# Optimization experiments

Hardware: AMD Instinct MI355X
Metric: run time of the kernel (lower is better)

The kernel has to match this reference:

```python
import jax, jax.numpy as jnp
import numpy as np

N, E, IN_DIM, HID, HEADS, OUT_DIM = 50000, 800000, 256, 32, 8, 64
NEG_SLOPE = 0.2  # PyG GATConv default


def segment_softmax(logits, seg, num_segments):
    # logits: [E, H], seg: [E] destination node ids. Self-loops guarantee no empty segment.
    m = jnp.full((num_segments, logits.shape[1]), -jnp.inf, logits.dtype).at[seg].max(logits)
    e = jnp.exp(logits - m[seg])
    s = jnp.zeros((num_segments, logits.shape[1]), logits.dtype).at[seg].add(e)
    return e / s[seg]


def gat_conv(x, src, dst, W, a_src, a_dst, b, heads, out_ch, concat):
    n = x.shape[0]
    h = (x @ W).reshape(n, heads, out_ch)                      # [N,H,C]
    alpha_src = jnp.einsum('nhc,hc->nh', h, a_src)             # [N,H]
    alpha_dst = jnp.einsum('nhc,hc->nh', h, a_dst)             # [N,H]
    logits = jax.nn.leaky_relu(alpha_src[src] + alpha_dst[dst], NEG_SLOPE)  # [E,H]
    alpha = segment_softmax(logits, dst, n)                    # [E,H]
    msg = alpha[:, :, None] * h[src]                           # [E,H,C]
    out = jnp.zeros((n, heads, out_ch), x.dtype).at[dst].add(msg)
    out = out.reshape(n, heads * out_ch) if concat else out.mean(axis=1)
    return out + b


def setup_inputs() -> dict:
    key = jax.random.key(0)
    ks = jax.random.split(key, 10)
    x = jax.random.normal(ks[0], (N, IN_DIM), dtype=jnp.float32)
    edge_index = jax.random.randint(ks[1], (2, E), 0, N, dtype=jnp.int64)
    s1 = 1.0 / np.sqrt(IN_DIM)
    s2 = 1.0 / np.sqrt(HID * HEADS)
    return {
        'x': x,
        'edge_index': edge_index,
        'W1': jax.random.normal(ks[2], (IN_DIM, HEADS * HID), dtype=jnp.float32) * s1,
        'a_src1': jax.random.normal(ks[3], (HEADS, HID), dtype=jnp.float32) * s1,
        'a_dst1': jax.random.normal(ks[4], (HEADS, HID), dtype=jnp.float32) * s1,
        'b1': jnp.zeros((HEADS * HID,), dtype=jnp.float32),
        'W2': jax.random.normal(ks[5], (HEADS * HID, OUT_DIM), dtype=jnp.float32) * s2,
        'a_src2': jax.random.normal(ks[6], (1, OUT_DIM), dtype=jnp.float32) * s2,
        'a_dst2': jax.random.normal(ks[7], (1, OUT_DIM), dtype=jnp.float32) * s2,
        'b2': jnp.zeros((OUT_DIM,), dtype=jnp.float32),
    }


def reference(x, edge_index, W1, a_src1, a_dst1, b1, W2, a_src2, a_dst2, b2):
    # add self-loops (PyG GATConv default add_self_loops=True)
    loops = jnp.arange(N, dtype=edge_index.dtype)
    src = jnp.concatenate([edge_index[0], loops])
    dst = jnp.concatenate([edge_index[1], loops])
    h = gat_conv(x, src, dst, W1, a_src1, a_dst1, b1, HEADS, HID, True)
    h = jax.nn.elu(h)  # dropout identity in eval mode
    out = gat_conv(h, src, dst, W2, a_src2, a_dst2, b2, 1, OUT_DIM, False)
    return out
```

## Files before the change

kernel.cpp:

```cpp
#include <hip/hip_runtime.h>
#include <hip/hip_bf16.h>

static constexpr int HEADS = 8;
static constexpr int D1 = 256;
static constexpr int ODIM = 64;
static constexpr float NEG = 0.2f;

typedef __attribute__((ext_vector_type(8))) short bf16x8;
typedef __attribute__((ext_vector_type(8))) unsigned short u16x8;
typedef __attribute__((ext_vector_type(4))) float f32x4;

__device__ __forceinline__ float lrelu(float x) { return fmaxf(x, NEG * x); }
__device__ __forceinline__ float elu1(float x) { return x > 0.f ? x : expm1f(x); }

__device__ __forceinline__ unsigned short f2bf(float f) {
  unsigned u = __float_as_uint(f);
  unsigned r = (u + 0x7fffu + ((u >> 16) & 1u)) >> 16;
  return (unsigned short)r;
}
__device__ __forceinline__ float bf2f(unsigned short h) {
  return __uint_as_float((unsigned)h << 16);
}

__device__ __forceinline__ void gload_lds16(const void* g, void* l) {
  __builtin_amdgcn_global_load_lds(
      (const __attribute__((address_space(1))) void*)g,
      (__attribute__((address_space(3))) void*)l, 16, 0, 0);
}

__global__ void k_hist_prep(const int* __restrict__ dst, int E, int TE,
                            int* __restrict__ deg, int* __restrict__ erank,
                            const float* __restrict__ W1, const float* __restrict__ W2,
                            unsigned short* __restrict__ BT1, unsigned short* __restrict__ B2T,
                            int HB) {
  int b = blockIdx.x;
  if (b < HB) {
    int i = b * 256 + threadIdx.x;
    if (i < TE) {
      int d = (i < E) ? dst[i] : (i - E);
      erank[i] = atomicAdd(&deg[d], 1);
    }
  } else {
    int t = (b - HB) * 256 + threadIdx.x;
    if (t < 65536) {
      int k = t >> 8, nn = t & 255;
      BT1[nn * 256 + k] = f2bf(W1[t]);
    } else if (t < 65536 + 16384) {
      int t2 = t - 65536;
      int k = t2 >> 6, nn = t2 & 63;
      B2T[nn * 256 + k] = f2bf(W2[t2]);
    }
  }
}

__global__ void k_scan_lb(const int* __restrict__ deg, int n, int TE,
                          int* __restrict__ offs,
                          int* __restrict__ tstate, int* __restrict__ ticket) {
  __shared__ int sm[256];
  __shared__ int sh[2];
  if (threadIdx.x == 0) sh[0] = atomicAdd(ticket, 1);
  __syncthreads();
  const int tile = sh[0];
  int i = tile * 256 + threadIdx.x;
  int v = (i < n) ? deg[i] : 0;
  sm[threadIdx.x] = v;
  __syncthreads();
  for (int off = 1; off < 256; off <<= 1) {
    int t = (threadIdx.x >= off) ? sm[threadIdx.x - off] : 0;
    __syncthreads();
    sm[threadIdx.x] += t;
    __syncthreads();
  }
  const int total = sm[255];
  if (threadIdx.x == 0) {
    if (tile == 0) {
      __hip_atomic_store(&tstate[0], (2 << 24) | total, __ATOMIC_RELEASE,
                         __HIP_MEMORY_SCOPE_AGENT);
      sh[1] = 0;
    } else {
      __hip_atomic_store(&tstate[tile], (1 << 24) | total, __ATOMIC_RELEASE,
                         __HIP_MEMORY_SCOPE_AGENT);
    }
  }
  __syncthreads();
  if (tile != 0) {
    if (threadIdx.x < 64) {
      const int lane = threadIdx.x;
      int running = 0;
      int wstart = tile - 1;
      for (;;) {
        int idx = wstart - lane;
        int st = (idx >= 0)
                     ? __hip_atomic_load(&tstate[idx], __ATOMIC_ACQUIRE,
                                         __HIP_MEMORY_SCOPE_AGENT)
                     : (2 << 24);
        if (__ballot(st == 0)) continue;
        unsigned long long pref = __ballot((st >> 24) == 2);
        int contrib;
        if (pref) {
          int flane = (int)__ffsll(pref) - 1;
          contrib = (lane <= flane) ? (st & 0xFFFFFF) : 0;
        } else {
          contrib = st & 0xFFFFFF;
        }
#pragma unroll
        for (int off2 = 1; off2 < 64; off2 <<= 1) contrib += __shfl_xor(contrib, off2);
        running += contrib;
        if (pref) break;
        wstart -= 64;
      }
      if (lane == 0) {
        sh[1] = running;
        __hip_atomic_store(&tstate[tile], (2 << 24) | (running + total),
                           __ATOMIC_RELEASE, __HIP_MEMORY_SCOPE_AGENT);
      }
    }
    __syncthreads();
  }
  const int base = sh[1];
  if (i < n) offs[i] = base + sm[threadIdx.x] - v;
  if (i == 0) offs[n] = TE;
}

__global__ __launch_bounds__(512) void k_gemm1s(
    const float* __restrict__ X,
    const unsigned short* __restrict__ BT,
    const float* __restrict__ a_src, const float* __restrict__ a_dst,
    unsigned short* __restrict__ h1b,
    float* __restrict__ asrc, float* __restrict__ adst,
    int M, int Mblk,
    const int* __restrict__ src, const int* __restrict__ dst, int E, int TE,
    const int* __restrict__ offs, const int* __restrict__ erank,
    int* __restrict__ csr_src) {
  __shared__ __align__(128) char As[16384];
  __shared__ __align__(128) char Bs[32768];
  if (blockIdx.x >= Mblk) {
    int i = (blockIdx.x - Mblk) * 512 + threadIdx.x;
    if (i < TE) {
      int s, d;
      if (i < E) { s = src[i]; d = dst[i]; } else { s = i - E; d = i - E; }
      csr_src[offs[d] + erank[i]] = s;
    }
    return;
  }
  const int tid = threadIdx.x;
  const int lane = tid & 63;
  const int wid = tid >> 6;
  const int bm = blockIdx.x * 128;
  const int wm = wid >> 2, wn = wid & 3;
  f32x4 acc[4][4] = {};
  float4 xv[2][2];
  auto loadX = [&](int kb) {
#pragma unroll
    for (int q = 0; q < 2; ++q) {
      int c = q * 512 + tid;
      int r = c >> 3, kc = c & 7;
      int gr = bm + r;
      xv[q][0] = make_float4(0.f, 0.f, 0.f, 0.f);
      xv[q][1] = xv[q][0];
      if (gr < M) {
        xv[q][0] = *(const float4*)&X[(size_t)gr * 256 + kb + kc * 8];
        xv[q][1] = *(const float4*)&X[(size_t)gr * 256 + kb + kc * 8 + 4];
      }
    }
  };
  loadX(0);
  for (int kb = 0; kb < 256; kb += 64) {
#pragma unroll
    for (int q = 0; q < 2; ++q) {
      int c = q * 512 + tid;
      int r = c >> 3, kc = c & 7;
      float vv[8] = {xv[q][0].x, xv[q][0].y, xv[q][0].z, xv[q][0].w,
                     xv[q][1].x, xv[q][1].y, xv[q][1].z, xv[q][1].w};
      u16x8 hv;
#pragma unroll
      for (int j = 0; j < 8; ++j) hv[j] = f2bf(vv[j]);
      *(u16x8*)(As + r * 128 + ((kc * 16) ^ ((r & 7) << 4))) = hv;
    }
#pragma unroll
    for (int q = 0; q < 4; ++q) {
      int c = q * 512 + tid;
      int col = c >> 3;
      int b = ((c & 7) * 16) ^ ((col & 7) << 4);
      gload_lds16(BT + (size_t)col * 256 + kb + (b >> 1),
                  Bs + (size_t)(q * 512 + (tid & ~63)) * 16);
    }
    __syncthreads();
    if (kb + 64 < 256) loadX(kb + 64);
#pragma unroll
    for (int ks = 0; ks < 2; ++ks) {
      bf16x8 af[4], bfr[4];
      int bb = ks * 64 + (lane >> 4) * 16;
#pragma unroll
      for (int mi = 0; mi < 4; ++mi) {
        int row = wm * 64 + mi * 16 + (lane & 15);
        af[mi] = *(const bf16x8*)(As + row * 128 + (bb ^ ((row & 7) << 4)));
      }
#pragma unroll
      for (int ni = 0; ni < 4; ++ni) {
        int col = wn * 64 + ni * 16 + (lane & 15);
        bfr[ni] = *(const bf16x8*)(Bs + col * 128 + (bb ^ ((col & 7) << 4)));
      }
#pragma unroll
      for (int mi = 0; mi < 4; ++mi)
#pragma unroll
        for (int ni = 0; ni < 4; ++ni)
          acc[mi][ni] = __builtin_amdgcn_mfma_f32_16x16x32_bf16(af[mi], bfr[ni],
                                                                acc[mi][ni], 0, 0, 0);
    }
    __syncthreads();
  }
  const int h0 = 2 * wn, h1h = 2 * wn + 1;
  const int cl = lane & 15;
  const float as0 = a_src[h0 * 32 + cl],      ad0 = a_dst[h0 * 32 + cl];
  const float as1 = a_src[h0 * 32 + 16 + cl], ad1 = a_dst[h0 * 32 + 16 + cl];
  const float as2 = a_src[h1h * 32 + cl],      ad2 = a_dst[h1h * 32 + cl];
  const float as3 = a_src[h1h * 32 + 16 + cl], ad3 = a_dst[h1h * 32 + 16 + cl];
#pragma unroll
  for (int mi = 0; mi < 4; ++mi) {
    int gr0 = bm + wm * 64 + mi * 16 + (lane >> 4) * 4;
#pragma unroll
    for (int j = 0; j < 4; ++j) {
      int gr = gr0 + j;
#pragma unroll
      for (int ni = 0; ni < 4; ++ni) {
        int gc = wn * 64 + ni * 16 + cl;
        if (gr < M) h1b[(size_t)gr * 256 + gc] = f2bf(acc[mi][ni][j]);
      }
      float ps0 = acc[mi][0][j] * as0 + acc[mi][1][j] * as1;
      float pd0 = acc[mi][0][j] * ad0 + acc[mi][1][j] * ad1;
      float ps1 = acc[mi][2][j] * as2 + acc[mi][3][j] * as3;
      float pd1 = acc[mi][2][j] * ad2 + acc[mi][3][j] * ad3;
#pragma unroll
      for (int off = 1; off < 16; off <<= 1) {
        ps0 += __shfl_xor(ps0, off);
        pd0 += __shfl_xor(pd0, off);
        ps1 += __shfl_xor(ps1, off);
        pd1 += __shfl_xor(pd1, off);
      }
      if (cl == 0 && gr < M) {
        asrc[gr * 8 + h0] = ps0;
        adst[gr * 8 + h0] = pd0;
        asrc[gr * 8 + h1h] = ps1;
        adst[gr * 8 + h1h] = pd1;
      }
    }
  }
}

__global__ __launch_bounds__(512) void k_gemm2(
    const unsigned short* __restrict__ A,
    const unsigned short* __restrict__ B2T,
    const float* __restrict__ a_src, const float* __restrict__ a_dst,
    unsigned short* __restrict__ C,
    float* __restrict__ asrc, float* __restrict__ adst,
    int M) {
  __shared__ __align__(128) char As[16384];
  __shared__ __align__(128) char Bs[8192];
  __shared__ float red[2][128][2];
  const int tid = threadIdx.x;
  const int lane = tid & 63;
  const int wid = tid >> 6;
  const int bm = blockIdx.x * 128;
  const int wm = wid >> 1, wn = wid & 1;
  f32x4 acc[2][2] = {};
  for (int kb = 0; kb < 256; kb += 64) {
#pragma unroll
    for (int q = 0; q < 2; ++q) {
      int c = q * 512 + tid;
      int r = c >> 3;
      int b = ((c & 7) * 16) ^ ((r & 7) << 4);
      gload_lds16(A + (size_t)(bm + r) * 256 + kb + (b >> 1),
                  As + (size_t)(q * 512 + (tid & ~63)) * 16);
    }
    {
      int c = tid;
      int col = c >> 3;
      int b = ((c & 7) * 16) ^ ((col & 7) << 4);
      gload_lds16(B2T + (size_t)col * 256 + kb + (b >> 1),
                  Bs + (size_t)(tid & ~63) * 16);
    }
    __syncthreads();
#pragma unroll
    for (int ks = 0; ks < 2; ++ks) {
      bf16x8 af[2], bfr[2];
      int bb = ks * 64 + (lane >> 4) * 16;
#pragma unroll
      for (int mi = 0; mi < 2; ++mi) {
        int row = wm * 32 + mi * 16 + (lane & 15);
        af[mi] = *(const bf16x8*)(As + row * 128 + (bb ^ ((row & 7) << 4)));
      }
#pragma unroll
      for (int ni = 0; ni < 2; ++ni) {
        int col = wn * 32 + ni * 16 + (lane & 15);
        bfr[ni] = *(const bf16x8*)(Bs + col * 128 + (bb ^ ((col & 7) << 4)));
      }
#pragma unroll
      for (int mi = 0; mi < 2; ++mi)
#pragma unroll
        for (int ni = 0; ni < 2; ++ni)
          acc[mi][ni] = __builtin_amdgcn_mfma_f32_16x16x32_bf16(af[mi], bfr[ni],
                                                                acc[mi][ni], 0, 0, 0);
    }
    __syncthreads();
  }
  const int cl = lane & 15;
  const float a_s0 = a_src[wn * 32 + cl],      a_d0 = a_dst[wn * 32 + cl];
  const float a_s1 = a_src[wn * 32 + 16 + cl], a_d1 = a_dst[wn * 32 + 16 + cl];
#pragma unroll
  for (int mi = 0; mi < 2; ++mi) {
    int rl0 = wm * 32 + mi * 16 + (lane >> 4) * 4;
#pragma unroll
    for (int j = 0; j < 4; ++j) {
      int rl = rl0 + j;
      int gr = bm + rl;
#pragma unroll
      for (int ni = 0; ni < 2; ++ni) {
        int gc = wn * 32 + ni * 16 + cl;
        if (gr < M) C[(size_t)gr * 64 + gc] = f2bf(acc[mi][ni][j]);
      }
      float ps = acc[mi][0][j] * a_s0 + acc[mi][1][j] * a_s1;
      float pd = acc[mi][0][j] * a_d0 + acc[mi][1][j] * a_d1;
#pragma unroll
      for (int off = 1; off < 16; off <<= 1) {
        ps += __shfl_xor(ps, off);
        pd += __shfl_xor(pd, off);
      }
      if (cl == 0) {
        red[wn][rl][0] = ps;
        red[wn][rl][1] = pd;
      }
    }
  }
  __syncthreads();
  if (tid < 128) {
    int gr = bm + tid;
    if (gr < M) {
      asrc[gr] = red[0][tid][0] + red[1][tid][0];
      adst[gr] = red[0][tid][1] + red[1][tid][1];
    }
  }
}

__global__ void k_agg1(const int* __restrict__ offs, const int* __restrict__ csr_src,
                       const unsigned short* __restrict__ h1b, const float* __restrict__ asrc,
                       const float* __restrict__ adst, const float* __restrict__ b1,
                       int n, unsigned short* __restrict__ helu) {
  int wave = (blockIdx.x * blockDim.x + threadIdx.x) >> 6;
  int lane = threadIdx.x & 63;
  if (wave >= n) return;
  int wv = __builtin_amdgcn_readfirstlane(wave);
  const int es = lane >> 5;
  const int cg = lane & 31;
  const int hh = cg >> 2;
  float ad = adst[wv * 8 + hh];
  int b = offs[wv], e2 = offs[wv + 1];
  float ssum = 0.f;
  float acc[8] = {};
  int i = b;
  for (; i + 7 < e2; i += 8) {
    int s[4];
#pragma unroll
    for (int u = 0; u < 4; ++u) s[u] = csr_src[i + 2 * u + es];
    u16x8 r[4];
    float as_[4];
#pragma unroll
    for (int u = 0; u < 4; ++u) {
      r[u] = *(const u16x8*)&h1b[(size_t)s[u] * D1 + cg * 8];
      as_[u] = asrc[s[u] * 8 + hh];
    }
#pragma unroll
    for (int u = 0; u < 4; ++u) {
      float w = __expf(lrelu(as_[u] + ad));
      ssum += w;
#pragma unroll
      for (int j = 0; j < 8; ++j) acc[j] += w * bf2f(r[u][j]);
    }
  }
  for (; i < e2; i += 2) {
    int idx = i + es;
    bool act = idx < e2;
    int s = csr_src[act ? idx : e2 - 1];
    u16x8 r = *(const u16x8*)&h1b[(size_t)s * D1 + cg * 8];
    float w = act ? __expf(lrelu(asrc[s * 8 + hh] + ad)) : 0.f;
    ssum += w;
#pragma unroll
    for (int j = 0; j < 8; ++j) acc[j] += w * bf2f(r[j]);
  }
  ssum += __shfl_xor(ssum, 32);
#pragma unroll
  for (int j = 0; j < 8; ++j) acc[j] += __shfl_xor(acc[j], 32);
  if (lane < 32) {
    float rr = 1.f / ssum;
    float4 bb0 = *(const float4*)&b1[cg * 8];
    float4 bb1 = *(const float4*)&b1[cg * 8 + 4];
    float bbv[8] = {bb0.x, bb0.y, bb0.z, bb0.w, bb1.x, bb1.y, bb1.z, bb1.w};
    u16x8 o;
#pragma unroll
    for (int j = 0; j < 8; ++j) o[j] = f2bf(elu1(acc[j] * rr + bbv[j]));
    *(u16x8*)&helu[(size_t)wave * D1 + cg * 8] = o;
  }
}

__global__ void k_agg2(const int* __restrict__ offs, const int* __restrict__ csr_src,
                       const unsigned short* __restrict__ h2b, const float* __restrict__ asrc,
                       const float* __restrict__ adst, const float* __restrict__ b2,
                       int n, float* __restrict__ out) {
  int wave = (blockIdx.x * blockDim.x + threadIdx.x) >> 6;
  int lane = threadIdx.x & 63;
  if (wave >= n) return;
  int wv = __builtin_amdgcn_readfirstlane(wave);
  float ad = adst[wv];
  int b = offs[wv], e2 = offs[wv + 1];
  const int es = lane >> 3;
  const int cg = lane & 7;
  float ssum = 0.f;
  float acc[8] = {};
  int i = b;
  for (; i + 15 < e2; i += 16) {
    int s0 = csr_src[i + es], s1 = csr_src[i + 8 + es];
    u16x8 r0 = *(const u16x8*)&h2b[(size_t)s0 * ODIM + cg * 8];
    u16x8 r1 = *(const u16x8*)&h2b[(size_t)s1 * ODIM + cg * 8];
    float a0 = asrc[s0], a1 = asrc[s1];
    float w0 = __expf(lrelu(a0 + ad));
    float w1 = __expf(lrelu(a1 + ad));
    ssum += w0 + w1;
#pragma unroll
    for (int j = 0; j < 8; ++j) acc[j] += w0 * bf2f(r0[j]) + w1 * bf2f(r1[j]);
  }
  for (; i < e2; i += 8) {
    int idx = i + es;
    bool act = idx < e2;
    int s = csr_src[act ? idx : e2 - 1];
    u16x8 r = *(const u16x8*)&h2b[(size_t)s * ODIM + cg * 8];
    float w = act ? __expf(lrelu(asrc[s] + ad)) : 0.f;
    ssum += w;
#pragma unroll
    for (int j = 0; j < 8; ++j) acc[j] += w * bf2f(r[j]);
  }
#pragma unroll
  for (int off = 8; off < 64; off <<= 1) {
    ssum += __shfl_xor(ssum, off);
#pragma unroll
    for (int j = 0; j < 8; ++j) acc[j] += __shfl_xor(acc[j], off);
  }
  if (lane < 8) {
    float r = 1.f / ssum;
    float4 bb0 = *(const float4*)&b2[cg * 8];
    float4 bb1 = *(const float4*)&b2[cg * 8 + 4];
    float4 o0, o1;
    o0.x = acc[0] * r + bb0.x; o0.y = acc[1] * r + bb0.y;
    o0.z = acc[2] * r + bb0.z; o0.w = acc[3] * r + bb0.w;
    o1.x = acc[4] * r + bb1.x; o1.y = acc[5] * r + bb1.y;
    o1.z = acc[6] * r + bb1.z; o1.w = acc[7] * r + bb1.w;
    *(float4*)&out[(size_t)wave * ODIM + cg * 8] = o0;
    *(float4*)&out[(size_t)wave * ODIM + cg * 8 + 4] = o1;
  }
}

extern "C" void kernel_launch(void* const* d_in, const int* in_sizes, int n_in,
                              void* d_out, int out_size, void* d_ws, size_t ws_size,
                              hipStream_t stream) {
  const float* x      = (const float*)d_in[0];
  const int* eidx     = (const int*)d_in[1];
  const float* W1     = (const float*)d_in[2];
  const float* asrc1w = (const float*)d_in[3];
  const float* adst1w = (const float*)d_in[4];
  const float* b1     = (const float*)d_in[5];
  const float* W2     = (const float*)d_in[6];
  const float* asrc2w = (const float*)d_in[7];
  const float* adst2w = (const float*)d_in[8];
  const float* b2     = (const float*)d_in[9];
  float* out = (float*)d_out;

  const int N = in_sizes[0] / D1;
  const int E = in_sizes[1] / 2;
  const int TE = E + N;
  const int* src = eidx;
  const int* dst = eidx + E;
  const int Mblk = (N + 127) / 128;
  const int Mpad = Mblk * 128;
  const int nb_n = (N + 255) / 256;
  const int nb_te = (TE + 255) / 256;
  const int nb_sc = (TE + 511) / 512;

  char* ws = (char*)d_ws;
  size_t off = 0;
  auto carve = [&](size_t bytes) -> char* {
    char* p = ws + off;
    off = (off + bytes + 255) & ~(size_t)255;
    return p;
  };
  unsigned short* helu = (unsigned short*)carve((size_t)Mpad * D1 * 2);
  unsigned short* h1b  = (unsigned short*)carve((size_t)Mpad * D1 * 2);
  unsigned short* h2b  = (unsigned short*)carve((size_t)N * ODIM * 2);
  unsigned short* BT1  = (unsigned short*)carve((size_t)256 * 256 * 2);
  unsigned short* B2T2 = (unsigned short*)carve((size_t)64 * 256 * 2);
  float* asrc1 = (float*)carve((size_t)N * HEADS * 4);
  float* adst1 = (float*)carve((size_t)N * HEADS * 4);
  float* asrc2 = (float*)carve((size_t)N * 4);
  float* adst2 = (float*)carve((size_t)N * 4);
  int* zr      = (int*)carve((size_t)(N + nb_n + 64) * 4);
  int* deg     = zr;
  int* tstate  = zr + N;
  int* ticket  = zr + N + nb_n;
  int* offs    = (int*)carve((size_t)(N + 1) * 4);
  int* erank   = (int*)carve((size_t)TE * 4);
  int* csr_src = (int*)carve((size_t)TE * 4);

  hipMemsetAsync(zr, 0, (size_t)(N + nb_n + 1) * 4, stream);
  {
    const int HB = nb_te;
    const int PB = (65536 + 16384) / 256;
    k_hist_prep<<<HB + PB, 256, 0, stream>>>(dst, E, TE, deg, erank, W1, W2, BT1, B2T2, HB);
  }
  k_scan_lb<<<nb_n, 256, 0, stream>>>(deg, N, TE, offs, tstate, ticket);

  k_gemm1s<<<Mblk + nb_sc, 512, 0, stream>>>(x, BT1, asrc1w, adst1w, h1b, asrc1, adst1,
                                             N, Mblk, src, dst, E, TE, offs, erank, csr_src);
  k_agg1<<<(N + 3) / 4, 256, 0, stream>>>(offs, csr_src, h1b, asrc1, adst1, b1, N, helu);

  k_gemm2<<<Mblk, 512, 0, stream>>>(helu, B2T2, asrc2w, adst2w, h2b, asrc2, adst2, N);
  k_agg2<<<(N + 3) / 4, 256, 0, stream>>>(offs, csr_src, h2b, asrc2, adst2, b2, N, out);
}
```

Measured before the change: 197.4 us.

## Fuse layer-1 aggregation with layer-2 GEMM and add nontemporal edge accesses

```diff
diff --git a/kernel.cpp b/kernel.cpp
--- a/kernel.cpp
+++ b/kernel.cpp
@@ -37,8 +37,9 @@
   if (b < HB) {
     int i = b * 256 + threadIdx.x;
     if (i < TE) {
-      int d = (i < E) ? dst[i] : (i - E);
-      erank[i] = atomicAdd(&deg[d], 1);
+      int d = (i < E) ? __builtin_nontemporal_load(&dst[i]) : (i - E);
+      int rk = atomicAdd(&deg[d], 1);
+      __builtin_nontemporal_store(rk, &erank[i]);
     }
   } else {
     int t = (b - HB) * 256 + threadIdx.x;
@@ -138,8 +139,12 @@
     int i = (blockIdx.x - Mblk) * 512 + threadIdx.x;
     if (i < TE) {
       int s, d;
-      if (i < E) { s = src[i]; d = dst[i]; } else { s = i - E; d = i - E; }
-      csr_src[offs[d] + erank[i]] = s;
+      if (i < E) {
+        s = __builtin_nontemporal_load(&src[i]);
+        d = __builtin_nontemporal_load(&dst[i]);
+      } else { s = i - E; d = i - E; }
+      int rk = __builtin_nontemporal_load(&erank[i]);
+      __builtin_nontemporal_store(s, &csr_src[offs[d] + rk]);
     }
     return;
   }
@@ -248,157 +253,101 @@
   }
 }
 
-__global__ __launch_bounds__(512) void k_gemm2(
-    const unsigned short* __restrict__ A,
+__global__ __launch_bounds__(256) void k_agg1f(
+    const int* __restrict__ offs, const int* __restrict__ csr_src,
+    const unsigned short* __restrict__ h1b,
+    const float* __restrict__ asrc1, const float* __restrict__ adst1,
+    const float* __restrict__ b1,
     const unsigned short* __restrict__ B2T,
-    const float* __restrict__ a_src, const float* __restrict__ a_dst,
-    unsigned short* __restrict__ C,
-    float* __restrict__ asrc, float* __restrict__ adst,
-    int M) {
-  __shared__ __align__(128) char As[16384];
-  __shared__ __align__(128) char Bs[8192];
-  __shared__ float red[2][128][2];
+    const float* __restrict__ a_src2, const float* __restrict__ a_dst2,
+    unsigned short* __restrict__ h2b,
+    float* __restrict__ asrc2, float* __restrict__ adst2,
+    int n) {
   const int tid = threadIdx.x;
   const int lane = tid & 63;
   const int wid = tid >> 6;
-  const int bm = blockIdx.x * 128;
-  const int wm = wid >> 1, wn = wid & 1;
-  f32x4 acc[2][2] = {};
-  for (int kb = 0; kb < 256; kb += 64) {
-#pragma unroll
-    for (int q = 0; q < 2; ++q) {
-      int c = q * 512 + tid;
-      int r = c >> 3;
-      int b = ((c & 7) * 16) ^ ((r & 7) << 4);
-      gload_lds16(A + (size_t)(bm + r) * 256 + kb + (b >> 1),
-                  As + (size_t)(q * 512 + (tid & ~63)) * 16);
-    }
-    {
-      int c = tid;
-      int col = c >> 3;
-      int b = ((c & 7) * 16) ^ ((col & 7) << 4);
-      gload_lds16(B2T + (size_t)col * 256 + kb + (b >> 1),
-                  Bs + (size_t)(tid & ~63) * 16);
-    }
-    __syncthreads();
-#pragma unroll
-    for (int ks = 0; ks < 2; ++ks) {
-      bf16x8 af[2], bfr[2];
-      int bb = ks * 64 + (lane >> 4) * 16;
-#pragma unroll
-      for (int mi = 0; mi < 2; ++mi) {
-        int row = wm * 32 + mi * 16 + (lane & 15);
-        af[mi] = *(const bf16x8*)(As + row * 128 + (bb ^ ((row & 7) << 4)));
-      }
-#pragma unroll
-      for (int ni = 0; ni < 2; ++ni) {
-        int col = wn * 32 + ni * 16 + (lane & 15);
-        bfr[ni] = *(const bf16x8*)(Bs + col * 128 + (bb ^ ((col & 7) << 4)));
-      }
-#pragma unroll
-      for (int mi = 0; mi < 2; ++mi)
-#pragma unroll
-        for (int ni = 0; ni < 2; ++ni)
-          acc[mi][ni] = __builtin_amdgcn_mfma_f32_16x16x32_bf16(af[mi], bfr[ni],
-                                                                acc[mi][ni], 0, 0, 0);
-    }
-    __syncthreads();
-  }
-  const int cl = lane & 15;
-  const float a_s0 = a_src[wn * 32 + cl],      a_d0 = a_dst[wn * 32 + cl];
-  const float a_s1 = a_src[wn * 32 + 16 + cl], a_d1 = a_dst[wn * 32 + 16 + cl];
-#pragma unroll
-  for (int mi = 0; mi < 2; ++mi) {
-    int rl0 = wm * 32 + mi * 16 + (lane >> 4) * 4;
-#pragma unroll
-    for (int j = 0; j < 4; ++j) {
-      int rl = rl0 + j;
-      int gr = bm + rl;
-#pragma unroll
-      for (int ni = 0; ni < 2; ++ni) {
-        int gc = wn * 32 + ni * 16 + cl;
-        if (gr < M) C[(size_t)gr * 64 + gc] = f2bf(acc[mi][ni][j]);
-      }
-      float ps = acc[mi][0][j] * a_s0 + acc[mi][1][j] * a_s1;
-      float pd = acc[mi][0][j] * a_d0 + acc[mi][1][j] * a_d1;
-#pragma unroll
-      for (int off = 1; off < 16; off <<= 1) {
-        ps += __shfl_xor(ps, off);
-        pd += __shfl_xor(pd, off);
-      }
-      if (cl == 0) {
-        red[wn][rl][0] = ps;
-        red[wn][rl][1] = pd;
-      }
-    }
-  }
-  __syncthreads();
-  if (tid < 128) {
-    int gr = bm + tid;
-    if (gr < M) {
-      asrc[gr] = red[0][tid][0] + red[1][tid][0];
-      adst[gr] = red[0][tid][1] + red[1][tid][1];
-    }
-  }
-}
-
-__global__ void k_agg1(const int* __restrict__ offs, const int* __restrict__ csr_src,
-                       const unsigned short* __restrict__ h1b, const float* __restrict__ asrc,
-                       const float* __restrict__ adst, const float* __restrict__ b1,
-                       int n, unsigned short* __restrict__ helu) {
-  int wave = (blockIdx.x * blockDim.x + threadIdx.x) >> 6;
-  int lane = threadIdx.x & 63;
-  if (wave >= n) return;
-  int wv = __builtin_amdgcn_readfirstlane(wave);
-  const int es = lane >> 5;
-  const int cg = lane & 31;
-  const int hh = cg >> 2;
-  float ad = adst[wv * 8 + hh];
-  int b = offs[wv], e2 = offs[wv + 1];
-  float ssum = 0.f;
-  float acc[8] = {};
-  int i = b;
-  for (; i + 7 < e2; i += 8) {
-    int s[4];
-#pragma unroll
-    for (int u = 0; u < 4; ++u) s[u] = csr_src[i + 2 * u + es];
-    u16x8 r[4];
-    float as_[4];
-#pragma unroll
-    for (int u = 0; u < 4; ++u) {
-      r[u] = *(const u16x8*)&h1b[(size_t)s[u] * D1 + cg * 8];
-      as_[u] = asrc[s[u] * 8 + hh];
-    }
-#pragma unroll
-    for (int u = 0; u < 4; ++u) {
-      float w = __expf(lrelu(as_[u] + ad));
-      ssum += w;
-#pragma unroll
-      for (int j = 0; j < 8; ++j) acc[j] += w * bf2f(r[u][j]);
-    }
-  }
-  for (; i < e2; i += 2) {
-    int idx = i + es;
-    bool act = idx < e2;
-    int s = csr_src[act ? idx : e2 - 1];
-    u16x8 r = *(const u16x8*)&h1b[(size_t)s * D1 + cg * 8];
-    float w = act ? __expf(lrelu(asrc[s * 8 + hh] + ad)) : 0.f;
-    ssum += w;
-#pragma unroll
-    for (int j = 0; j < 8; ++j) acc[j] += w * bf2f(r[j]);
-  }
-  ssum += __shfl_xor(ssum, 32);
-#pragma unroll
-  for (int j = 0; j < 8; ++j) acc[j] += __shfl_xor(acc[j], 32);
-  if (lane < 32) {
-    float rr = 1.f / ssum;
-    float4 bb0 = *(const float4*)&b1[cg * 8];
-    float4 bb1 = *(const float4*)&b1[cg * 8 + 4];
-    float bbv[8] = {bb0.x, bb0.y, bb0.z, bb0.w, bb1.x, bb1.y, bb1.z, bb1.w};
-    u16x8 o;
-#pragma unroll
-    for (int j = 0; j < 8; ++j) o[j] = f2bf(elu1(acc[j] * rr + bbv[j]));
-    *(u16x8*)&helu[(size_t)wave * D1 + cg * 8] = o;
+  const int nb = blockIdx.x * 64 + wid * 16;
+  const int hi = lane >> 4;
+  const int nt = lane & 15;
+  const int node = nb + nt;
+  const bool valid = node < n;
+  int b = 0, e = 0;
+  if (valid) { b = offs[node]; e = offs[node + 1]; }
+  float ad[8];
+  {
+    int an = valid ? node : 0;
+    float4 a0 = *(const float4*)&adst1[an * 8];
+    float4 a1 = *(const float4*)&adst1[an * 8 + 4];
+    ad[0] = a0.x; ad[1] = a0.y; ad[2] = a0.z; ad[3] = a0.w;
+    ad[4] = a1.x; ad[5] = a1.y; ad[6] = a1.z; ad[7] = a1.w;
+  }
+  float ssum[8] = {};
+  float acc[64] = {};
+  for (int it = 0;; ++it) {
+    bool act = (b + it) < e;
+    if (!__any(act)) break;
+    if (act) {
+      int s = csr_src[b + it];
+      float4 s0 = *(const float4*)&asrc1[s * 8];
+      float4 s1 = *(const float4*)&asrc1[s * 8 + 4];
+      float asv[8] = {s0.x, s0.y, s0.z, s0.w, s1.x, s1.y, s1.z, s1.w};
+      u16x8 r[8];
+#pragma unroll
+      for (int kk = 0; kk < 8; ++kk)
+        r[kk] = *(const u16x8*)&h1b[(size_t)s * 256 + kk * 32 + hi * 8];
+#pragma unroll
+      for (int kk = 0; kk < 8; ++kk) {
+        float w = __expf(lrelu(asv[kk] + ad[kk]));
+        ssum[kk] += w;
+#pragma unroll
+        for (int j = 0; j < 8; ++j) acc[kk * 8 + j] += w * bf2f(r[kk][j]);
+      }
+    }
+  }
+  bf16x8 af[8];
+#pragma unroll
+  for (int kk = 0; kk < 8; ++kk) {
+    float rr = ssum[kk] > 0.f ? 1.f / ssum[kk] : 0.f;
+    int cb = kk * 32 + hi * 8;
+    float4 b0 = *(const float4*)&b1[cb];
+    float4 b1v = *(const float4*)&b1[cb + 4];
+    float bb[8] = {b0.x, b0.y, b0.z, b0.w, b1v.x, b1v.y, b1v.z, b1v.w};
+#pragma unroll
+    for (int j = 0; j < 8; ++j)
+      af[kk][j] = (short)f2bf(elu1(acc[kk * 8 + j] * rr + bb[j]));
+  }
+  f32x4 c2[4] = {};
+#pragma unroll
+  for (int kk = 0; kk < 8; ++kk) {
+#pragma unroll
+    for (int ni = 0; ni < 4; ++ni) {
+      bf16x8 bf = *(const bf16x8*)&B2T[(size_t)(ni * 16 + nt) * 256 + kk * 32 + hi * 8];
+      c2[ni] = __builtin_amdgcn_mfma_f32_16x16x32_bf16(af[kk], bf, c2[ni], 0, 0, 0);
+    }
+  }
+  float a2s[4], a2d[4];
+#pragma unroll
+  for (int ni = 0; ni < 4; ++ni) {
+    a2s[ni] = a_src2[ni * 16 + nt];
+    a2d[ni] = a_dst2[ni * 16 + nt];
+  }
+#pragma unroll
+  for (int j = 0; j < 4; ++j) {
+    int row = nb + hi * 4 + j;
+    bool rv = row < n;
+    float ps = 0.f, pd = 0.f;
+#pragma unroll
+    for (int ni = 0; ni < 4; ++ni) {
+      if (rv) h2b[(size_t)row * 64 + ni * 16 + nt] = f2bf(c2[ni][j]);
+      ps += a2s[ni] * c2[ni][j];
+      pd += a2d[ni] * c2[ni][j];
+    }
+#pragma unroll
+    for (int off = 1; off < 16; off <<= 1) {
+      ps += __shfl_xor(ps, off);
+      pd += __shfl_xor(pd, off);
+    }
+    if (nt == 0 && rv) { asrc2[row] = ps; adst2[row] = pd; }
   }
 }
 
@@ -483,6 +432,7 @@
   const int nb_n = (N + 255) / 256;
   const int nb_te = (TE + 255) / 256;
   const int nb_sc = (TE + 511) / 512;
+  const int nb_f  = (N + 63) / 64;
 
   char* ws = (char*)d_ws;
   size_t off = 0;
@@ -491,7 +441,6 @@
     off = (off + bytes + 255) & ~(size_t)255;
     return p;
   };
-  unsigned short* helu = (unsigned short*)carve((size_t)Mpad * D1 * 2);
   unsigned short* h1b  = (unsigned short*)carve((size_t)Mpad * D1 * 2);
   unsigned short* h2b  = (unsigned short*)carve((size_t)N * ODIM * 2);
   unsigned short* BT1  = (unsigned short*)carve((size_t)256 * 256 * 2);
@@ -518,8 +467,9 @@
 
   k_gemm1s<<<Mblk + nb_sc, 512, 0, stream>>>(x, BT1, asrc1w, adst1w, h1b, asrc1, adst1,
                                              N, Mblk, src, dst, E, TE, offs, erank, csr_src);
-  k_agg1<<<(N + 3) / 4, 256, 0, stream>>>(offs, csr_src, h1b, asrc1, adst1, b1, N, helu);
-
-  k_gemm2<<<Mblk, 512, 0, stream>>>(helu, B2T2, asrc2w, adst2w, h2b, asrc2, adst2, N);
+
+  k_agg1f<<<nb_f, 256, 0, stream>>>(offs, csr_src, h1b, asrc1, adst1, b1,
+                                    B2T2, asrc2w, adst2w, h2b, asrc2, adst2, N);
+
   k_agg2<<<(N + 3) / 4, 256, 0, stream>>>(offs, csr_src, h2b, asrc2, adst2, b2, N, out);
 }
```

Result: slower. 252.4 us (+27.9%).

## Partition layer-1 aggregation by head slice per XCD for L2 locality

Applied to the files above, without the earlier changes.

```diff
diff --git a/kernel.cpp b/kernel.cpp
--- a/kernel.cpp
+++ b/kernel.cpp
@@ -26,6 +26,12 @@
   __builtin_amdgcn_global_load_lds(
       (const __attribute__((address_space(1))) void*)g,
       (__attribute__((address_space(3))) void*)l, 16, 0, 0);
+}
+
+__device__ __forceinline__ int xcd_id() {
+  int x;
+  asm volatile("s_getreg_b32 %0, hwreg(20, 0, 32)" : "=s"(x));
+  return x & 7;
 }
 
 __global__ void k_hist_prep(const int* __restrict__ dst, int E, int TE,
@@ -37,8 +43,9 @@
   if (b < HB) {
     int i = b * 256 + threadIdx.x;
     if (i < TE) {
-      int d = (i < E) ? dst[i] : (i - E);
-      erank[i] = atomicAdd(&deg[d], 1);
+      int d = (i < E) ? __builtin_nontemporal_load(&dst[i]) : (i - E);
+      int rk = atomicAdd(&deg[d], 1);
+      __builtin_nontemporal_store(rk, &erank[i]);
     }
   } else {
     int t = (b - HB) * 256 + threadIdx.x;
@@ -138,8 +145,12 @@
     int i = (blockIdx.x - Mblk) * 512 + threadIdx.x;
     if (i < TE) {
       int s, d;
-      if (i < E) { s = src[i]; d = dst[i]; } else { s = i - E; d = i - E; }
-      csr_src[offs[d] + erank[i]] = s;
+      if (i < E) {
+        s = __builtin_nontemporal_load(&src[i]);
+        d = __builtin_nontemporal_load(&dst[i]);
+      } else { s = i - E; d = i - E; }
+      int rk = __builtin_nontemporal_load(&erank[i]);
+      __builtin_nontemporal_store(s, &csr_src[offs[d] + rk]);
     }
     return;
   }
@@ -244,6 +255,78 @@
         asrc[gr * 8 + h1h] = ps1;
         adst[gr * 8 + h1h] = pd1;
       }
+    }
+  }
+}
+
+__global__ __launch_bounds__(256) void k_agg1(
+    const int* __restrict__ offs, const int* __restrict__ csr_src,
+    const unsigned short* __restrict__ h1b, const float* __restrict__ asrc,
+    const float* __restrict__ adst, const float* __restrict__ b1,
+    int n, int cps, int* __restrict__ sticket,
+    unsigned short* __restrict__ helu) {
+  __shared__ int sh_chunk, sh_slice;
+  if (threadIdx.x == 0) {
+    int sl = xcd_id();
+    int got = -1, gsl = 0;
+    for (int o = 0; o < 8; ++o) {
+      int s2 = (sl + o) & 7;
+      int t = atomicAdd(&sticket[s2], 1);
+      if (t < cps) { got = t; gsl = s2; break; }
+    }
+    sh_chunk = got;
+    sh_slice = gsl;
+  }
+  __syncthreads();
+  const int chunk = sh_chunk;
+  const int h = sh_slice;
+  if (chunk < 0) return;
+  const int lane = threadIdx.x & 63;
+  const int wid = threadIdx.x >> 6;
+  const int es = lane >> 2;
+  const int cq = lane & 3;
+  const int cb = h * 32 + cq * 8;
+  float4 bbv0 = *(const float4*)&b1[cb];
+  float4 bbv1 = *(const float4*)&b1[cb + 4];
+  float bb[8] = {bbv0.x, bbv0.y, bbv0.z, bbv0.w, bbv1.x, bbv1.y, bbv1.z, bbv1.w};
+  for (int t = 0; t < 16; ++t) {
+    const int node = chunk * 64 + wid * 16 + t;
+    if (node >= n) break;
+    const int b = offs[node], e2 = offs[node + 1];
+    const float ad = adst[node * 8 + h];
+    float ssum = 0.f;
+    float acc[8] = {};
+    int i = b;
+    for (; i + 15 < e2; i += 16) {
+      int s = csr_src[i + es];
+      u16x8 r = *(const u16x8*)&h1b[(size_t)s * D1 + cb];
+      float w = __expf(lrelu(asrc[s * 8 + h] + ad));
+      ssum += w;
+#pragma unroll
+      for (int j = 0; j < 8; ++j) acc[j] += w * bf2f(r[j]);
+    }
+    if (i < e2) {
+      int idx = i + es;
+      bool act = idx < e2;
+      int s = csr_src[act ? idx : e2 - 1];
+      u16x8 r = *(const u16x8*)&h1b[(size_t)s * D1 + cb];
+      float w = act ? __expf(lrelu(asrc[s * 8 + h] + ad)) : 0.f;
+      ssum += w;
+#pragma unroll
+      for (int j = 0; j < 8; ++j) acc[j] += w * bf2f(r[j]);
+    }
+#pragma unroll
+    for (int off = 4; off < 64; off <<= 1) {
+      ssum += __shfl_xor(ssum, off);
+#pragma unroll
+      for (int j = 0; j < 8; ++j) acc[j] += __shfl_xor(acc[j], off);
+    }
+    if (es == 0) {
+      float rr = 1.f / ssum;
+      u16x8 o;
+#pragma unroll
+      for (int j = 0; j < 8; ++j) o[j] = f2bf(elu1(acc[j] * rr + bb[j]));
+      *(u16x8*)&helu[(size_t)node * D1 + cb] = o;
     }
   }
 }
@@ -339,66 +422,6 @@
       asrc[gr] = red[0][tid][0] + red[1][tid][0];
       adst[gr] = red[0][tid][1] + red[1][tid][1];
     }
-  }
-}
-
-__global__ void k_agg1(const int* __restrict__ offs, const int* __restrict__ csr_src,
-                       const unsigned short* __restrict__ h1b, const float* __restrict__ asrc,
-                       const float* __restrict__ adst, const float* __restrict__ b1,
-                       int n, unsigned short* __restrict__ helu) {
-  int wave = (blockIdx.x * blockDim.x + threadIdx.x) >> 6;
-  int lane = threadIdx.x & 63;
-  if (wave >= n) return;
-  int wv = __builtin_amdgcn_readfirstlane(wave);
-  const int es = lane >> 5;
-  const int cg = lane & 31;
-  const int hh = cg >> 2;
-  float ad = adst[wv * 8 + hh];
-  int b = offs[wv], e2 = offs[wv + 1];
-  float ssum = 0.f;
-  float acc[8] = {};
-  int i = b;
-  for (; i + 7 < e2; i += 8) {
-    int s[4];
-#pragma unroll
-    for (int u = 0; u < 4; ++u) s[u] = csr_src[i + 2 * u + es];
-    u16x8 r[4];
-    float as_[4];
-#pragma unroll
-    for (int u = 0; u < 4; ++u) {
-      r[u] = *(const u16x8*)&h1b[(size_t)s[u] * D1 + cg * 8];
-      as_[u] = asrc[s[u] * 8 + hh];
-    }
-#pragma unroll
-    for (int u = 0; u < 4; ++u) {
-      float w = __expf(lrelu(as_[u] + ad));
-      ssum += w;
-#pragma unroll
-      for (int j = 0; j < 8; ++j) acc[j] += w * bf2f(r[u][j]);
-    }
-  }
-  for (; i < e2; i += 2) {
-    int idx = i + es;
-    bool act = idx < e2;
-    int s = csr_src[act ? idx : e2 - 1];
-    u16x8 r = *(const u16x8*)&h1b[(size_t)s * D1 + cg * 8];
-    float w = act ? __expf(lrelu(asrc[s * 8 + hh] + ad)) : 0.f;
-    ssum += w;
-#pragma unroll
-    for (int j = 0; j < 8; ++j) acc[j] += w * bf2f(r[j]);
-  }
-  ssum += __shfl_xor(ssum, 32);
-#pragma unroll
-  for (int j = 0; j < 8; ++j) acc[j] += __shfl_xor(acc[j], 32);
-  if (lane < 32) {
-    float rr = 1.f / ssum;
-    float4 bb0 = *(const float4*)&b1[cg * 8];
-    float4 bb1 = *(const float4*)&b1[cg * 8 + 4];
-    float bbv[8] = {bb0.x, bb0.y, bb0.z, bb0.w, bb1.x, bb1.y, bb1.z, bb1.w};
-    u16x8 o;
-#pragma unroll
-    for (int j = 0; j < 8; ++j) o[j] = f2bf(elu1(acc[j] * rr + bbv[j]));
-    *(u16x8*)&helu[(size_t)wave * D1 + cg * 8] = o;
   }
 }
 
@@ -483,6 +506,7 @@
   const int nb_n = (N + 255) / 256;
   const int nb_te = (TE + 255) / 256;
   const int nb_sc = (TE + 511) / 512;
+  const int cps = (N + 63) / 64;
 
   char* ws = (char*)d_ws;
   size_t off = 0;
@@ -504,11 +528,12 @@
   int* deg     = zr;
   int* tstate  = zr + N;
   int* ticket  = zr + N + nb_n;
+  int* sticket = zr + N + nb_n + 1;
   int* offs    = (int*)carve((size_t)(N + 1) * 4);
   int* erank   = (int*)carve((size_t)TE * 4);
   int* csr_src = (int*)carve((size_t)TE * 4);
 
-  hipMemsetAsync(zr, 0, (size_t)(N + nb_n + 1) * 4, stream);
+  hipMemsetAsync(zr, 0, (size_t)(N + nb_n + 16) * 4, stream);
   {
     const int HB = nb_te;
     const int PB = (65536 + 16384) / 256;
@@ -518,7 +543,9 @@
 
   k_gemm1s<<<Mblk + nb_sc, 512, 0, stream>>>(x, BT1, asrc1w, adst1w, h1b, asrc1, adst1,
                                              N, Mblk, src, dst, E, TE, offs, erank, csr_src);
-  k_agg1<<<(N + 3) / 4, 256, 0, stream>>>(offs, csr_src, h1b, asrc1, adst1, b1, N, helu);
+
+  k_agg1<<<8 * cps, 256, 0, stream>>>(offs, csr_src, h1b, asrc1, adst1, b1,
+                                      N, cps, sticket, helu);
 
   k_gemm2<<<Mblk, 512, 0, stream>>>(helu, B2T2, asrc2w, adst2w, h2b, asrc2, adst2, N);
   k_agg2<<<(N + 3) / 4, 256, 0, stream>>>(offs, csr_src, h2b, asrc2, adst2, b2, N, out);
```

Result: slower. 352.1 us (+78.4%).
